# Performance work log

Hardware: AMD Instinct MI355X
Metric: run time of the kernel (lower is better)

## Reference

```python
import jax, jax.numpy as jnp
import numpy as np

L = 80
INTERVAL = 5
NCPT = int(np.ceil(L / INTERVAL)) + 1          # 17
INTERVAL2 = 1 if INTERVAL == 1 else L - (NCPT - 2) * INTERVAL  # 5
N = (L + 1) ** 2                                # 6561
REPEATS = np.array([2 * l + 1 for l in range(L + 1)])  # static, sums to N


def setup_inputs() -> dict:
    key = jax.random.key(0)
    k1, k2 = jax.random.split(key)
    in_ch, out_ch, batch = 64, 64, 32
    x = jax.random.normal(k1, (batch, in_ch, N), dtype=jnp.float32)
    stdv = 1.0 / np.sqrt(in_ch * (L + 1))
    weight = jax.random.uniform(k2, (in_ch, out_ch, NCPT, 1),
                                dtype=jnp.float32, minval=-stdv, maxval=stdv)
    return {"x": x, "weight": weight}


def reference(x, weight):
    # interpolation coefficients (constants, match torch buffers)
    l0 = jnp.tile(jnp.arange(INTERVAL, dtype=jnp.float32) / INTERVAL,
                  (NCPT - 2, 1))                       # (ncpt-2, interval)
    l1 = (jnp.arange(INTERVAL2 + 1, dtype=jnp.float32) / INTERVAL2)[None, :]  # (1, interval2+1)

    in_ch, out_ch = weight.shape[0], weight.shape[1]
    # linear interpolation between anchor points
    w1 = ((1.0 - l0) * weight[:, :, :-2, :] + l0 * weight[:, :, 1:-1, :])
    w1 = w1.reshape(in_ch, out_ch, -1)                 # (in, out, (ncpt-2)*interval)
    w2 = ((1.0 - l1) * weight[:, :, -2:-1, :] + l1 * weight[:, :, -1:, :])
    w2 = w2.reshape(in_ch, out_ch, -1)                 # (in, out, interval2+1)
    w_l = jnp.concatenate([w1, w2], axis=2)            # (in, out, L+1)

    # expand per-degree coeff to 2l+1 orders -> (in, out, (L+1)^2)
    w = jnp.repeat(w_l, REPEATS, axis=2, total_repeat_length=N)

    # per-position channel mixing: sum over in_ch, no (b,in,out,N) intermediate
    return jnp.einsum('bin,ion->bon', x, w)
```

## Files before the change

### kernel.cpp

```cpp
#include <hip/hip_runtime.h>
#include <hip/hip_bf16.h>


#define NTOT 6561
#define NL   81
#define CH   64
#define NSLOTS 451
#define WTB_BYTES (NL * CH * CH * 2)

typedef __attribute__((ext_vector_type(8))) short bf16x8;
typedef __attribute__((ext_vector_type(4))) float f32x4;

__global__ __launch_bounds__(256) void interp_bf16(const float* __restrict__ w,
                                                   __hip_bfloat16* __restrict__ wtb) {
  int idx = blockIdx.x * 256 + threadIdx.x;
  int l = idx >> 12;
  int o = (idx >> 6) & 63;
  int i = idx & 63;
  int cp; float f;
  if (l < 75) { cp = l / 5; f = (float)(l - cp * 5) * 0.2f; }
  else        { cp = 15;    f = (float)(l - 75) * 0.2f; }
  const float* wp = w + (size_t)(i * 64 + o) * 17 + cp;
  float v = (1.0f - f) * wp[0] + f * wp[1];
  wtb[(size_t)l * 4096 + o * 64 + i] = __float2bfloat16(v);
}

__global__ __launch_bounds__(256) void shconv_mfma(const float* __restrict__ x,
                                                   const __hip_bfloat16* __restrict__ wtb,
                                                   float* __restrict__ out) {
  const int s = blockIdx.x * 4 + (threadIdx.x >> 6);
  if (s >= NSLOTS) return;
  const int b = blockIdx.y;

  int g = 0;
  while (g < 10 && 4 * (g + 1) * (g + 2) <= s) ++g;
  const int r = s - 4 * g * (g + 1);
  const int l = 8 * g + r / (g + 1);
  const int c = r - (l - 8 * g) * (g + 1);
  const int P = 2 * l + 1;

  const int lane = threadIdx.x & 63;
  const int m  = lane & 15;
  const int kg = lane >> 4;

  const int p = c * 16 + m;
  const int pl = (p < P) ? p : (P - 1);
  const size_t nbase = (size_t)l * l;
  const float* xb = x + (size_t)b * CH * NTOT + nbase + pl;

  float xraw[16];
#pragma unroll
  for (int ks = 0; ks < 2; ++ks)
#pragma unroll
    for (int j = 0; j < 8; ++j)
      xraw[ks * 8 + j] = xb[(size_t)(ks * 32 + kg * 8 + j) * NTOT];

  bf16x8 bfrag[2];
#pragma unroll
  for (int ks = 0; ks < 2; ++ks)
#pragma unroll
    for (int j = 0; j < 8; ++j) {
      __hip_bfloat16 h = __float2bfloat16(xraw[ks * 8 + j]);
      bfrag[ks][j] = *reinterpret_cast<short*>(&h);
    }

  const __hip_bfloat16* wl = wtb + (size_t)l * 4096;
  f32x4 acc[4];
#pragma unroll
  for (int t = 0; t < 4; ++t) acc[t] = (f32x4)(0.0f);

#pragma unroll
  for (int ks = 0; ks < 2; ++ks) {
#pragma unroll
    for (int t = 0; t < 4; ++t) {
      const int o = t * 16 + m;
      const int i0 = ks * 32 + kg * 8;
      bf16x8 afrag = *reinterpret_cast<const bf16x8*>(wl + (size_t)o * 64 + i0);
      acc[t] = __builtin_amdgcn_mfma_f32_16x16x32_bf16(afrag, bfrag[ks], acc[t], 0, 0, 0);
    }
  }

  if (p < P) {
    float* ob = out + (size_t)b * CH * NTOT + nbase + p;
#pragma unroll
    for (int t = 0; t < 4; ++t)
#pragma unroll
      for (int rg = 0; rg < 4; ++rg) {
        const int o = t * 16 + kg * 4 + rg;
        ob[(size_t)o * NTOT] = acc[t][rg];
      }
  }
}

__global__ __launch_bounds__(192) void shconv_fallback(const float* __restrict__ x,
                                                       const float* __restrict__ w,
                                                       float* __restrict__ out) {
  __shared__ float wl[2][64][64];
  const int l1 = blockIdx.x;
  const int l2 = 80 - l1;
  const int P1 = 2 * l1 + 1;
  const int P2 = (l1 == 40) ? 0 : 2 * l2 + 1;
  int cp1, cp2; float f1, f2;
  if (l1 < 75) { cp1 = l1 / 5; f1 = (float)(l1 - cp1 * 5) * 0.2f; }
  else         { cp1 = 15;     f1 = (float)(l1 - 75) * 0.2f; }
  if (l2 < 75) { cp2 = l2 / 5; f2 = (float)(l2 - cp2 * 5) * 0.2f; }
  else         { cp2 = 15;     f2 = (float)(l2 - 75) * 0.2f; }
  const int tid = threadIdx.x;
  for (int e = tid; e < 8192; e += 192) {
    int sel = e >> 12, rr = e & 4095, i = rr >> 6, o = rr & 63;
    int cp = sel ? cp2 : cp1;
    float f = sel ? f2 : f1;
    const float* wp = w + (size_t)(i * 64 + o) * 17 + cp;
    wl[sel][i][o] = (1.0f - f) * wp[0] + f * wp[1];
  }
  __syncthreads();
  const int Ptot = P1 + P2;
  if (tid >= Ptot) return;
  int sel, l, p;
  if (tid < P1) { sel = 0; l = l1; p = tid; }
  else          { sel = 1; l = l2; p = tid - P1; }
  const size_t nidx = (size_t)(l * l) + p;
  const int b0 = blockIdx.y, b1 = b0 + 16;
  const float* x0 = x + (size_t)b0 * CH * NTOT + nidx;
  const float* x1 = x + (size_t)b1 * CH * NTOT + nidx;
  float acc0[64], acc1[64];
#pragma unroll
  for (int o = 0; o < 64; ++o) { acc0[o] = 0.f; acc1[o] = 0.f; }
  const float* wbase = &wl[sel][0][0];
#pragma unroll 4
  for (int i = 0; i < 64; ++i) {
    float xv0 = x0[(size_t)i * NTOT];
    float xv1 = x1[(size_t)i * NTOT];
    const float* wr = wbase + i * 64;
#pragma unroll
    for (int o = 0; o < 64; o += 4) {
      float4 wv = *(const float4*)(wr + o);
      acc0[o]     = fmaf(xv0, wv.x, acc0[o]);
      acc0[o + 1] = fmaf(xv0, wv.y, acc0[o + 1]);
      acc0[o + 2] = fmaf(xv0, wv.z, acc0[o + 2]);
      acc0[o + 3] = fmaf(xv0, wv.w, acc0[o + 3]);
      acc1[o]     = fmaf(xv1, wv.x, acc1[o]);
      acc1[o + 1] = fmaf(xv1, wv.y, acc1[o + 1]);
      acc1[o + 2] = fmaf(xv1, wv.z, acc1[o + 2]);
      acc1[o + 3] = fmaf(xv1, wv.w, acc1[o + 3]);
    }
  }
  float* o0 = out + (size_t)b0 * CH * NTOT + nidx;
  float* o1 = out + (size_t)b1 * CH * NTOT + nidx;
#pragma unroll
  for (int o = 0; o < 64; ++o) {
    o0[(size_t)o * NTOT] = acc0[o];
    o1[(size_t)o * NTOT] = acc1[o];
  }
}

extern "C" void kernel_launch(void* const* d_in, const int* in_sizes, int n_in,
                              void* d_out, int out_size, void* d_ws, size_t ws_size,
                              hipStream_t stream) {
  const float* x = (const float*)d_in[0];
  const float* w = (const float*)d_in[1];
  float* out = (float*)d_out;

  if (ws_size >= (size_t)WTB_BYTES && d_ws != nullptr) {
    __hip_bfloat16* wtb = (__hip_bfloat16*)d_ws;
    hipLaunchKernelGGL(interp_bf16, dim3(1296), dim3(256), 0, stream, w, wtb);
    hipLaunchKernelGGL(shconv_mfma, dim3(113, 32), dim3(256), 0, stream, x, wtb, out);
  } else {
    hipLaunchKernelGGL(shconv_fallback, dim3(41, 16), dim3(192), 0, stream, x, w, out);
  }
}
```

Before: 37.50 us.

## Stage x and output tiles through LDS with 64-position chunks per block

Replaces the per-wave 16-position slot mapping with blocks covering a 64-position chunk of one degree l. Input x is loaded cooperatively into shared memory, with each wave reading 64 consecutive positions per channel, so global reads are wider and more contiguous. Results are staged through shared memory before being written out the same way. This adds two barriers and LDS traffic, and it wastes lanes in chunks that are only partly filled.

```diff
diff --git a/kernel.cpp b/kernel.cpp
--- a/kernel.cpp
+++ b/kernel.cpp
@@ -5,7 +5,7 @@
 #define NTOT 6561
 #define NL   81
 #define CH   64
-#define NSLOTS 451
+#define NSLOT64 147
 #define WTB_BYTES (NL * CH * CH * 2)
 
 typedef __attribute__((ext_vector_type(8))) short bf16x8;
@@ -25,70 +25,89 @@
   wtb[(size_t)l * 4096 + o * 64 + i] = __float2bfloat16(v);
 }
 
-__global__ __launch_bounds__(256) void shconv_mfma(const float* __restrict__ x,
-                                                   const __hip_bfloat16* __restrict__ wtb,
-                                                   float* __restrict__ out) {
-  const int s = blockIdx.x * 4 + (threadIdx.x >> 6);
-  if (s >= NSLOTS) return;
+__global__ __launch_bounds__(256, 4) void shconv_mfma3(const float* __restrict__ x,
+                                                       const __hip_bfloat16* __restrict__ wtb,
+                                                       float* __restrict__ out) {
+  __shared__ float xs[64][66];
+  __shared__ float os[64][66];
+
+  const int s = blockIdx.x;
   const int b = blockIdx.y;
+  int l, c;
+  if (s < 32)      { l = s;                  c = 0; }
+  else if (s < 96) { l = 32 + ((s - 32) >> 1); c = (s - 32) & 1; }
+  else             { l = 64 + (s - 96) / 3;    c = (s - 96) % 3; }
+  const int P  = 2 * l + 1;
+  const int n0 = l * l + c * 64;
+  const int Pc = min(64, P - c * 64);
 
-  int g = 0;
-  while (g < 10 && 4 * (g + 1) * (g + 2) <= s) ++g;
-  const int r = s - 4 * g * (g + 1);
-  const int l = 8 * g + r / (g + 1);
-  const int c = r - (l - 8 * g) * (g + 1);
-  const int P = 2 * l + 1;
+  const int tid  = threadIdx.x;
+  const int wv   = tid >> 6;
+  const int lane = tid & 63;
 
-  const int lane = threadIdx.x & 63;
-  const int m  = lane & 15;
-  const int kg = lane >> 4;
+  {
+    int n = n0 + lane;
+    if (n > NTOT - 1) n = NTOT - 1;
+    const float* xb = x + (size_t)b * CH * NTOT + n;
+#pragma unroll
+    for (int r = 0; r < 16; ++r) {
+      const int ch = r * 4 + wv;
+      xs[lane][ch] = xb[(size_t)ch * NTOT];
+    }
+  }
+  __syncthreads();
 
-  const int p = c * 16 + m;
-  const int pl = (p < P) ? p : (P - 1);
-  const size_t nbase = (size_t)l * l;
-  const float* xb = x + (size_t)b * CH * NTOT + nbase + pl;
+  const int m   = lane & 15;
+  const int kg  = lane >> 4;
+  const int pc0 = wv * 16;
+  if (pc0 < Pc) {
+    const int p = pc0 + m;
 
-  float xraw[16];
+    bf16x8 bf[2];
 #pragma unroll
-  for (int ks = 0; ks < 2; ++ks)
+    for (int ks = 0; ks < 2; ++ks) {
+      const int i0 = ks * 32 + kg * 8;
 #pragma unroll
-    for (int j = 0; j < 8; ++j)
-      xraw[ks * 8 + j] = xb[(size_t)(ks * 32 + kg * 8 + j) * NTOT];
-
-  bf16x8 bfrag[2];
-#pragma unroll
-  for (int ks = 0; ks < 2; ++ks)
-#pragma unroll
-    for (int j = 0; j < 8; ++j) {
-      __hip_bfloat16 h = __float2bfloat16(xraw[ks * 8 + j]);
-      bfrag[ks][j] = *reinterpret_cast<short*>(&h);
+      for (int u = 0; u < 4; ++u) {
+        float2 v = *(const float2*)&xs[p][i0 + 2 * u];
+        __hip_bfloat16 h0 = __float2bfloat16(v.x);
+        __hip_bfloat16 h1 = __float2bfloat16(v.y);
+        bf[ks][2 * u]     = *reinterpret_cast<short*>(&h0);
+        bf[ks][2 * u + 1] = *reinterpret_cast<short*>(&h1);
+      }
     }
 
-  const __hip_bfloat16* wl = wtb + (size_t)l * 4096;
-  f32x4 acc[4];
+    const __hip_bfloat16* wl = wtb + (size_t)l * 4096;
+    f32x4 acc[4];
 #pragma unroll
-  for (int t = 0; t < 4; ++t) acc[t] = (f32x4)(0.0f);
+    for (int t = 0; t < 4; ++t) acc[t] = (f32x4)(0.0f);
 
 #pragma unroll
-  for (int ks = 0; ks < 2; ++ks) {
+    for (int ks = 0; ks < 2; ++ks) {
 #pragma unroll
-    for (int t = 0; t < 4; ++t) {
-      const int o = t * 16 + m;
-      const int i0 = ks * 32 + kg * 8;
-      bf16x8 afrag = *reinterpret_cast<const bf16x8*>(wl + (size_t)o * 64 + i0);
-      acc[t] = __builtin_amdgcn_mfma_f32_16x16x32_bf16(afrag, bfrag[ks], acc[t], 0, 0, 0);
+      for (int t = 0; t < 4; ++t) {
+        const int o  = t * 16 + m;
+        const int i0 = ks * 32 + kg * 8;
+        bf16x8 afrag = *reinterpret_cast<const bf16x8*>(wl + (size_t)o * 64 + i0);
+        acc[t] = __builtin_amdgcn_mfma_f32_16x16x32_bf16(afrag, bf[ks], acc[t], 0, 0, 0);
+      }
     }
-  }
 
-  if (p < P) {
-    float* ob = out + (size_t)b * CH * NTOT + nbase + p;
 #pragma unroll
     for (int t = 0; t < 4; ++t)
 #pragma unroll
-      for (int rg = 0; rg < 4; ++rg) {
-        const int o = t * 16 + kg * 4 + rg;
-        ob[(size_t)o * NTOT] = acc[t][rg];
-      }
+      for (int rg = 0; rg < 4; ++rg)
+        os[t * 16 + kg * 4 + rg][pc0 + m] = acc[t][rg];
+  }
+  __syncthreads();
+
+  if (lane < Pc) {
+    float* ob = out + (size_t)b * CH * NTOT + n0 + lane;
+#pragma unroll
+    for (int r = 0; r < 16; ++r) {
+      const int o = r * 4 + wv;
+      ob[(size_t)o * NTOT] = os[o][lane];
+    }
   }
 }
 
@@ -164,7 +183,7 @@
   if (ws_size >= (size_t)WTB_BYTES && d_ws != nullptr) {
     __hip_bfloat16* wtb = (__hip_bfloat16*)d_ws;
     hipLaunchKernelGGL(interp_bf16, dim3(1296), dim3(256), 0, stream, w, wtb);
-    hipLaunchKernelGGL(shconv_mfma, dim3(113, 32), dim3(256), 0, stream, x, wtb, out);
+    hipLaunchKernelGGL(shconv_mfma3, dim3(NSLOT64, 32), dim3(256), 0, stream, x, wtb, out);
   } else {
     hipLaunchKernelGGL(shconv_fallback, dim3(41, 16), dim3(192), 0, stream, x, w, out);
   }
```

Result: slower. 44.67 us (+19.1%).

## Stage x and output through LDS in contiguous 128-position windows for high degrees

Applied to the files above, without the earlier changes.

For positions from 1024 up, each block now loads a contiguous 128-position window of x with float4 loads into LDS as bf16. It then walks the degree segments inside the window, issuing MFMAs per 16-column tile with the matching per-degree weights. Results are staged in LDS and written back with float4 stores, aiming to make global traffic coalesced instead of per-degree scattered 16-wide slices. Low degrees keep the old per-slot path. The cost is extra LDS, two barriers, and some wasted MFMA tiles where a tile straddles degree boundaries.

```diff
diff --git a/kernel.cpp b/kernel.cpp
--- a/kernel.cpp
+++ b/kernel.cpp
@@ -5,8 +5,10 @@
 #define NTOT 6561
 #define NL   81
 #define CH   64
-#define NSLOTS 451
 #define WTB_BYTES (NL * CH * CH * 2)
+#define NWINB 44
+#define GXA   20
+#define GXT   (NWINB + GXA)
 
 typedef __attribute__((ext_vector_type(8))) short bf16x8;
 typedef __attribute__((ext_vector_type(4))) float f32x4;
@@ -25,70 +27,169 @@
   wtb[(size_t)l * 4096 + o * 64 + i] = __float2bfloat16(v);
 }
 
-__global__ __launch_bounds__(256) void shconv_mfma(const float* __restrict__ x,
-                                                   const __hip_bfloat16* __restrict__ wtb,
-                                                   float* __restrict__ out) {
-  const int s = blockIdx.x * 4 + (threadIdx.x >> 6);
-  if (s >= NSLOTS) return;
-  const int b = blockIdx.y;
-
-  int g = 0;
-  while (g < 10 && 4 * (g + 1) * (g + 2) <= s) ++g;
-  const int r = s - 4 * g * (g + 1);
-  const int l = 8 * g + r / (g + 1);
-  const int c = r - (l - 8 * g) * (g + 1);
-  const int P = 2 * l + 1;
-
-  const int lane = threadIdx.x & 63;
-  const int m  = lane & 15;
-  const int kg = lane >> 4;
-
-  const int p = c * 16 + m;
-  const int pl = (p < P) ? p : (P - 1);
-  const size_t nbase = (size_t)l * l;
-  const float* xb = x + (size_t)b * CH * NTOT + nbase + pl;
-
-  float xraw[16];
-#pragma unroll
-  for (int ks = 0; ks < 2; ++ks)
-#pragma unroll
-    for (int j = 0; j < 8; ++j)
-      xraw[ks * 8 + j] = xb[(size_t)(ks * 32 + kg * 8 + j) * NTOT];
-
-  bf16x8 bfrag[2];
-#pragma unroll
-  for (int ks = 0; ks < 2; ++ks)
-#pragma unroll
-    for (int j = 0; j < 8; ++j) {
-      __hip_bfloat16 h = __float2bfloat16(xraw[ks * 8 + j]);
-      bfrag[ks][j] = *reinterpret_cast<short*>(&h);
-    }
-
-  const __hip_bfloat16* wl = wtb + (size_t)l * 4096;
-  f32x4 acc[4];
-#pragma unroll
-  for (int t = 0; t < 4; ++t) acc[t] = (f32x4)(0.0f);
-
-#pragma unroll
-  for (int ks = 0; ks < 2; ++ks) {
-#pragma unroll
-    for (int t = 0; t < 4; ++t) {
-      const int o = t * 16 + m;
-      const int i0 = ks * 32 + kg * 8;
-      bf16x8 afrag = *reinterpret_cast<const bf16x8*>(wl + (size_t)o * 64 + i0);
-      acc[t] = __builtin_amdgcn_mfma_f32_16x16x32_bf16(afrag, bfrag[ks], acc[t], 0, 0, 0);
-    }
-  }
-
-  if (p < P) {
-    float* ob = out + (size_t)b * CH * NTOT + nbase + p;
-#pragma unroll
-    for (int t = 0; t < 4; ++t)
-#pragma unroll
-      for (int rg = 0; rg < 4; ++rg) {
-        const int o = t * 16 + kg * 4 + rg;
-        ob[(size_t)o * NTOT] = acc[t][rg];
-      }
+__device__ __forceinline__ int isqrt_dev(int n) {
+  int r = (int)sqrtf((float)n);
+  while ((r + 1) * (r + 1) <= n) ++r;
+  while (r * r > n) --r;
+  return r;
+}
+
+__global__ __launch_bounds__(256) void shconv_fused(const float* __restrict__ x,
+                                                    const __hip_bfloat16* __restrict__ wtb,
+                                                    float* __restrict__ out) {
+  __shared__ __hip_bfloat16 xs[128][66];
+  __shared__ float os[64][132];
+
+  const int tid  = threadIdx.x;
+  const int wv   = tid >> 6;
+  const int lane = tid & 63;
+  const int m    = lane & 15;
+  const int kg   = lane >> 4;
+  const int b    = blockIdx.y;
+
+  if (blockIdx.x < NWINB) {
+    const int n0    = 1024 + (int)blockIdx.x * 128;
+    const int valid = min(128, NTOT - n0);
+
+    {
+      const float* xb = x + (size_t)b * CH * NTOT;
+      const int qs  = lane & 31;
+      const int chb = (wv << 4) + (lane >> 5);
+      int np = n0 + 4 * qs;
+      int lp = 4 * qs;
+      if (np > NTOT - 4) {
+        lp -= np - (NTOT - 4);
+        np = NTOT - 4;
+      }
+#pragma unroll
+      for (int u = 0; u < 8; ++u) {
+        const int ch = chb + (u << 1);
+        float4 v;
+        __builtin_memcpy(&v, xb + (size_t)ch * NTOT + np, 16);
+        xs[lp + 0][ch] = __float2bfloat16(v.x);
+        xs[lp + 1][ch] = __float2bfloat16(v.y);
+        xs[lp + 2][ch] = __float2bfloat16(v.z);
+        xs[lp + 3][ch] = __float2bfloat16(v.w);
+      }
+    }
+    __syncthreads();
+
+    int lcur = isqrt_dev(n0);
+    int pa = 0;
+    while (pa < valid) {
+      int pb = (lcur + 1) * (lcur + 1) - n0;
+      if (pb > valid) pb = valid;
+      const __hip_bfloat16* wl = wtb + (size_t)lcur * 4096;
+#pragma unroll
+      for (int kk = 0; kk < 2; ++kk) {
+        const int k0 = (wv * 2 + kk) * 16;
+        if (k0 + 16 > pa && k0 < pb) {
+          const int p = k0 + m;
+          bf16x8 bf[2];
+#pragma unroll
+          for (int ks = 0; ks < 2; ++ks) {
+            const int i0 = ks * 32 + kg * 8;
+            __builtin_memcpy(&bf[ks], &xs[p][i0], 16);
+          }
+          f32x4 acc[4];
+#pragma unroll
+          for (int t = 0; t < 4; ++t) acc[t] = (f32x4)(0.0f);
+#pragma unroll
+          for (int ks = 0; ks < 2; ++ks) {
+#pragma unroll
+            for (int t = 0; t < 4; ++t) {
+              const int o  = t * 16 + m;
+              const int i0 = ks * 32 + kg * 8;
+              bf16x8 afrag = *reinterpret_cast<const bf16x8*>(wl + (size_t)o * 64 + i0);
+              acc[t] = __builtin_amdgcn_mfma_f32_16x16x32_bf16(afrag, bf[ks], acc[t], 0, 0, 0);
+            }
+          }
+          if (p >= pa && p < pb) {
+#pragma unroll
+            for (int t = 0; t < 4; ++t)
+#pragma unroll
+              for (int rg = 0; rg < 4; ++rg)
+                os[t * 16 + kg * 4 + rg][p] = acc[t][rg];
+          }
+        }
+      }
+      pa = pb;
+      ++lcur;
+    }
+    __syncthreads();
+
+    {
+      float* ob = out + (size_t)b * CH * NTOT;
+      const int s4  = (lane & 31) * 4;
+      const int obc = (wv << 4) + (lane >> 5);
+#pragma unroll
+      for (int u = 0; u < 8; ++u) {
+        const int o = obc + (u << 1);
+        if (s4 + 4 <= valid) {
+          float4 v = *(const float4*)&os[o][s4];
+          __builtin_memcpy(ob + (size_t)o * NTOT + n0 + s4, &v, 16);
+        } else {
+          for (int vv = 0; vv < 4; ++vv)
+            if (s4 + vv < valid)
+              ob[(size_t)o * NTOT + n0 + s4 + vv] = os[o][s4 + vv];
+        }
+      }
+    }
+  } else {
+    const int s = ((int)blockIdx.x - NWINB) * 4 + wv;
+    int l, c;
+    if (s < 8)       { l = s;                    c = 0; }
+    else if (s < 24) { l = 8 + ((s - 8) >> 1);   c = (s - 8) & 1; }
+    else if (s < 48) { l = 16 + (s - 24) / 3;    c = (s - 24) % 3; }
+    else             { l = 24 + ((s - 48) >> 2); c = (s - 48) & 3; }
+    const int P = 2 * l + 1;
+
+    const int p  = c * 16 + m;
+    const int pl = (p < P) ? p : (P - 1);
+    const size_t nbase = (size_t)l * l;
+    const float* xb = x + (size_t)b * CH * NTOT + nbase + pl;
+
+    float xraw[16];
+#pragma unroll
+    for (int ks = 0; ks < 2; ++ks)
+#pragma unroll
+      for (int j = 0; j < 8; ++j)
+        xraw[ks * 8 + j] = xb[(size_t)(ks * 32 + kg * 8 + j) * NTOT];
+
+    bf16x8 bf[2];
+#pragma unroll
+    for (int ks = 0; ks < 2; ++ks)
+#pragma unroll
+      for (int j = 0; j < 8; ++j) {
+        __hip_bfloat16 h = __float2bfloat16(xraw[ks * 8 + j]);
+        bf[ks][j] = *reinterpret_cast<short*>(&h);
+      }
+
+    const __hip_bfloat16* wl = wtb + (size_t)l * 4096;
+    f32x4 acc[4];
+#pragma unroll
+    for (int t = 0; t < 4; ++t) acc[t] = (f32x4)(0.0f);
+#pragma unroll
+    for (int ks = 0; ks < 2; ++ks) {
+#pragma unroll
+      for (int t = 0; t < 4; ++t) {
+        const int o  = t * 16 + m;
+        const int i0 = ks * 32 + kg * 8;
+        bf16x8 afrag = *reinterpret_cast<const bf16x8*>(wl + (size_t)o * 64 + i0);
+        acc[t] = __builtin_amdgcn_mfma_f32_16x16x32_bf16(afrag, bf[ks], acc[t], 0, 0, 0);
+      }
+    }
+
+    if (p < P) {
+      float* ob = out + (size_t)b * CH * NTOT + nbase + p;
+#pragma unroll
+      for (int t = 0; t < 4; ++t)
+#pragma unroll
+        for (int rg = 0; rg < 4; ++rg) {
+          const int o = t * 16 + kg * 4 + rg;
+          ob[(size_t)o * NTOT] = acc[t][rg];
+        }
+    }
   }
 }
 
@@ -164,7 +265,7 @@
   if (ws_size >= (size_t)WTB_BYTES && d_ws != nullptr) {
     __hip_bfloat16* wtb = (__hip_bfloat16*)d_ws;
     hipLaunchKernelGGL(interp_bf16, dim3(1296), dim3(256), 0, stream, w, wtb);
-    hipLaunchKernelGGL(shconv_mfma, dim3(113, 32), dim3(256), 0, stream, x, wtb, out);
+    hipLaunchKernelGGL(shconv_fused, dim3(GXT, 32), dim3(256), 0, stream, x, wtb, out);
   } else {
     hipLaunchKernelGGL(shconv_fallback, dim3(41, 16), dim3(192), 0, stream, x, w, out);
   }
```

Result: slower. 46.27 us (+23.4%).

## Process four batches per wavefront with reused weight fragments and double-buffered loads

Applied to the files above, without the earlier changes.

Each wavefront now handles four batch items for one slot instead of one. The bf16 weight fragments are loaded once and kept in registers for all four, and x loads for the next batch are issued before the current batch's MFMA and stores, using two register buffers. This cuts repeated weight loads and aims to hide global load latency. In exchange it uses more registers and launches a quarter as many waves, which may lower occupancy on a memory-bound kernel.

```diff
diff --git a/kernel.cpp b/kernel.cpp
--- a/kernel.cpp
+++ b/kernel.cpp
@@ -25,12 +25,54 @@
   wtb[(size_t)l * 4096 + o * 64 + i] = __float2bfloat16(v);
 }
 
-__global__ __launch_bounds__(256) void shconv_mfma(const float* __restrict__ x,
+__device__ __forceinline__ void load_item(const float* __restrict__ xb,
+                                          float (&xr)[16], int kg) {
+#pragma unroll
+  for (int ks = 0; ks < 2; ++ks)
+#pragma unroll
+    for (int j = 0; j < 8; ++j)
+      xr[ks * 8 + j] = xb[(size_t)(ks * 32 + kg * 8 + j) * NTOT];
+}
+
+__device__ __forceinline__ void compute_store(const float (&xr)[16],
+                                              const bf16x8 (&afrag)[2][4],
+                                              float* __restrict__ ob,
+                                              bool act, int kg) {
+  bf16x8 bf[2];
+#pragma unroll
+  for (int ks = 0; ks < 2; ++ks)
+#pragma unroll
+    for (int j = 0; j < 8; ++j) {
+      __hip_bfloat16 h = __float2bfloat16(xr[ks * 8 + j]);
+      bf[ks][j] = *reinterpret_cast<short*>(&h);
+    }
+  f32x4 acc[4];
+#pragma unroll
+  for (int t = 0; t < 4; ++t) acc[t] = (f32x4)(0.0f);
+#pragma unroll
+  for (int ks = 0; ks < 2; ++ks)
+#pragma unroll
+    for (int t = 0; t < 4; ++t)
+      acc[t] = __builtin_amdgcn_mfma_f32_16x16x32_bf16(afrag[ks][t], bf[ks], acc[t], 0, 0, 0);
+  if (act) {
+#pragma unroll
+    for (int t = 0; t < 4; ++t)
+#pragma unroll
+      for (int rg = 0; rg < 4; ++rg)
+        ob[(size_t)(t * 16 + kg * 4 + rg) * NTOT] = acc[t][rg];
+  }
+}
+
+__global__ __launch_bounds__(256) void shconv_pipe(const float* __restrict__ x,
                                                    const __hip_bfloat16* __restrict__ wtb,
                                                    float* __restrict__ out) {
-  const int s = blockIdx.x * 4 + (threadIdx.x >> 6);
-  if (s >= NSLOTS) return;
-  const int b = blockIdx.y;
+  const int wv   = threadIdx.x >> 6;
+  const int lane = threadIdx.x & 63;
+  const int m    = lane & 15;
+  const int kg   = lane >> 4;
+  const int wg   = (int)blockIdx.x * 4 + wv;
+  const int s    = wg >> 3;
+  const int bq   = wg & 7;
 
   int g = 0;
   while (g < 10 && 4 * (g + 1) * (g + 2) <= s) ++g;
@@ -39,57 +81,39 @@
   const int c = r - (l - 8 * g) * (g + 1);
   const int P = 2 * l + 1;
 
-  const int lane = threadIdx.x & 63;
-  const int m  = lane & 15;
-  const int kg = lane >> 4;
+  const int p  = c * 16 + m;
+  const int pl = (p < P) ? p : (P - 1);
+  const bool act = (p < P);
+  const size_t nbase = (size_t)l * l;
 
-  const int p = c * 16 + m;
-  const int pl = (p < P) ? p : (P - 1);
-  const size_t nbase = (size_t)l * l;
-  const float* xb = x + (size_t)b * CH * NTOT + nbase + pl;
-
-  float xraw[16];
+  const __hip_bfloat16* wl = wtb + (size_t)l * 4096;
+  bf16x8 afrag[2][4];
 #pragma unroll
   for (int ks = 0; ks < 2; ++ks)
 #pragma unroll
-    for (int j = 0; j < 8; ++j)
-      xraw[ks * 8 + j] = xb[(size_t)(ks * 32 + kg * 8 + j) * NTOT];
+    for (int t = 0; t < 4; ++t)
+      afrag[ks][t] = *reinterpret_cast<const bf16x8*>(
+          wl + (size_t)(t * 16 + m) * 64 + ks * 32 + kg * 8);
 
-  bf16x8 bfrag[2];
-#pragma unroll
-  for (int ks = 0; ks < 2; ++ks)
-#pragma unroll
-    for (int j = 0; j < 8; ++j) {
-      __hip_bfloat16 h = __float2bfloat16(xraw[ks * 8 + j]);
-      bfrag[ks][j] = *reinterpret_cast<short*>(&h);
-    }
+  const int b0 = bq * 4;
+  const float* xp0 = x + (size_t)(b0 + 0) * CH * NTOT + nbase + pl;
+  const float* xp1 = x + (size_t)(b0 + 1) * CH * NTOT + nbase + pl;
+  const float* xp2 = x + (size_t)(b0 + 2) * CH * NTOT + nbase + pl;
+  const float* xp3 = x + (size_t)(b0 + 3) * CH * NTOT + nbase + pl;
+  float* op0 = out + (size_t)(b0 + 0) * CH * NTOT + nbase + p;
+  float* op1 = out + (size_t)(b0 + 1) * CH * NTOT + nbase + p;
+  float* op2 = out + (size_t)(b0 + 2) * CH * NTOT + nbase + p;
+  float* op3 = out + (size_t)(b0 + 3) * CH * NTOT + nbase + p;
 
-  const __hip_bfloat16* wl = wtb + (size_t)l * 4096;
-  f32x4 acc[4];
-#pragma unroll
-  for (int t = 0; t < 4; ++t) acc[t] = (f32x4)(0.0f);
-
-#pragma unroll
-  for (int ks = 0; ks < 2; ++ks) {
-#pragma unroll
-    for (int t = 0; t < 4; ++t) {
-      const int o = t * 16 + m;
-      const int i0 = ks * 32 + kg * 8;
-      bf16x8 afrag = *reinterpret_cast<const bf16x8*>(wl + (size_t)o * 64 + i0);
-      acc[t] = __builtin_amdgcn_mfma_f32_16x16x32_bf16(afrag, bfrag[ks], acc[t], 0, 0, 0);
-    }
-  }
-
-  if (p < P) {
-    float* ob = out + (size_t)b * CH * NTOT + nbase + p;
-#pragma unroll
-    for (int t = 0; t < 4; ++t)
-#pragma unroll
-      for (int rg = 0; rg < 4; ++rg) {
-        const int o = t * 16 + kg * 4 + rg;
-        ob[(size_t)o * NTOT] = acc[t][rg];
-      }
-  }
+  float xrA[16], xrB[16];
+  load_item(xp0, xrA, kg);
+  load_item(xp1, xrB, kg);
+  compute_store(xrA, afrag, op0, act, kg);
+  load_item(xp2, xrA, kg);
+  compute_store(xrB, afrag, op1, act, kg);
+  load_item(xp3, xrB, kg);
+  compute_store(xrA, afrag, op2, act, kg);
+  compute_store(xrB, afrag, op3, act, kg);
 }
 
 __global__ __launch_bounds__(192) void shconv_fallback(const float* __restrict__ x,
@@ -164,7 +188,7 @@
   if (ws_size >= (size_t)WTB_BYTES && d_ws != nullptr) {
     __hip_bfloat16* wtb = (__hip_bfloat16*)d_ws;
     hipLaunchKernelGGL(interp_bf16, dim3(1296), dim3(256), 0, stream, w, wtb);
-    hipLaunchKernelGGL(shconv_mfma, dim3(113, 32), dim3(256), 0, stream, x, wtb, out);
+    hipLaunchKernelGGL(shconv_pipe, dim3(902), dim3(256), 0, stream, x, wtb, out);
   } else {
     hipLaunchKernelGGL(shconv_fallback, dim3(41, 16), dim3(192), 0, stream, x, w, out);
   }
```

After: 54.79 us. 46.1% more time.
